# Performance work log

Hardware: AMD Instinct MI355X
Metric: run time of the kernel (lower is better)

Reference implementation:

```python
import jax, jax.numpy as jnp
from jax import lax
import numpy as np

NEG = -1e30  # safe log-space -inf for fp32 (avoids inf-inf NaNs)
EPS = 1e-7   # keras.backend.epsilon()


def setup_inputs() -> dict:
    key = jax.random.key(0)
    k1, k2 = jax.random.split(key)
    B, T, C, L = 512, 512, 96, 64
    y_true = jax.random.randint(k1, (B, L), 0, C - 1, dtype=jnp.int64)  # labels in [0, C-2]
    # y_pred mimics softmax output: positive, rows sum to 1
    logits = jax.random.uniform(k2, (B, T, C), dtype=jnp.float32)
    y_pred = logits / jnp.sum(logits, axis=-1, keepdims=True)
    return {"y_true": y_true, "y_pred": y_pred}


def _ctc_batch_cost(y_true, y_pred):
    # Faithful to keras.backend.ctc_batch_cost with full input/label lengths
    # and blank index = num_classes - 1.
    B, T, C = y_pred.shape
    L = y_true.shape[1]
    blank = C - 1
    S = 2 * L + 1  # extended label length: blanks interleaved

    logp = jnp.log(y_pred + EPS)  # [B, T, C]

    # extended label sequence: blank, l0, blank, l1, ..., blank
    ext = jnp.full((B, S), blank, dtype=y_true.dtype).at[:, 1::2].set(y_true)  # [B, S]

    # log-probs of extended labels at every time step: [T, B, S]
    lp = jnp.take_along_axis(
        logp, jnp.broadcast_to(ext[:, None, :], (B, T, S)), axis=2
    ).transpose(1, 0, 2)

    # skip transition (s-2 -> s) allowed iff ext[s] != blank and ext[s] != ext[s-2]
    skip = jnp.concatenate(
        [jnp.zeros((B, 2), dtype=bool),
         (ext[:, 2:] != blank) & (ext[:, 2:] != ext[:, :-2])],
        axis=1,
    )  # [B, S]

    # init: alpha_0(0) = logp(blank), alpha_0(1) = logp(l0)
    alpha0 = jnp.full((B, S), NEG, dtype=logp.dtype)
    alpha0 = alpha0.at[:, 0].set(lp[0, :, 0]).at[:, 1].set(lp[0, :, 1])

    def step(alpha, lp_t):
        s1 = jnp.pad(alpha[:, :-1], ((0, 0), (1, 0)), constant_values=NEG)
        s2 = jnp.pad(alpha[:, :-2], ((0, 0), (2, 0)), constant_values=NEG)
        a = jnp.logaddexp(alpha, s1)
        a = jnp.where(skip, jnp.logaddexp(a, s2), a)
        return a + lp_t, None

    alpha, _ = lax.scan(step, alpha0, lp[1:])
    loss = -jnp.logaddexp(alpha[:, -1], alpha[:, -2])  # [B]
    return loss[:, None]  # [B, 1], matching ctc_batch_cost


def reference(y_true, y_pred):
    return _ctc_batch_cost(y_true, y_pred)
```

## Files before the change

### kernel.cpp

```cpp
#include <hip/hip_runtime.h>
#include <math.h>


constexpr int Bv = 512;
constexpr int Tv = 512;
constexpr int Cv = 96;
constexpr int Lv = 64;
constexpr int BLANK = Cv - 1;
constexpr float EPSf = 1e-7f;
constexpr int RING = 24;

__device__ __forceinline__ float dpp_wave_shr1(float x) {
    return __int_as_float(
        __builtin_amdgcn_update_dpp(0, __float_as_int(x), 0x138, 0xf, 0xf, true));
}

template <int CTRL>
__device__ __forceinline__ float dpp_maxf(float m) {
    return fmaxf(m, __int_as_float(
        __builtin_amdgcn_update_dpp(0, __float_as_int(m), CTRL, 0xf, 0xf, true)));
}

__global__ void __launch_bounds__(64) ctc_fwd(const int* __restrict__ y_true,
                                              const float* __restrict__ y_pred,
                                              float* __restrict__ out) {
    const int b = blockIdx.x;
    const int l = threadIdx.x;
    const float* __restrict__ yp = y_pred + (size_t)b * (Tv * Cv);

    const int lab   = y_true[b * Lv + l];
    const int labm1 = __shfl_up(lab, 1);
    const bool skip = (l > 0) && (lab != labm1);
    const bool lane0 = (l == 0);

    float a0 = lane0 ? (yp[BLANK] + EPSf) : 0.0f;
    float a1 = lane0 ? (yp[lab]  + EPSf) : 0.0f;
    float a2 = 0.0f;
    int   e_acc = 0;

    float fb[RING], fl[RING];
#pragma unroll
    for (int i = 0; i < RING; ++i) {
        int t = 1 + i;
        fb[i] = yp[t * Cv + BLANK];
        fl[i] = yp[t * Cv + lab];
    }

    auto step = [&](int t, int slot) {
        float pb = fb[slot] + EPSf;
        float pl = fl[slot] + EPSf;
        int tp = t + RING;
        tp = (tp > Tv - 1) ? (Tv - 1) : tp;
        fb[slot] = yp[tp * Cv + BLANK];
        fl[slot] = yp[tp * Cv + lab];

        float a1p = dpp_wave_shr1(a1);
        float na0 = (a0 + a1p) * pb;
        float s1  = a0 + a1 + (skip ? a1p : 0.0f);
        float na1 = s1 * pl;
        float na2 = (a2 + a1) * pb;
        a0 = na0; a1 = na1; a2 = na2;
    };

    auto renorm = [&]() {
        float m = fmaxf(fmaxf(a0, a1), a2);
        m = dpp_maxf<0x111>(m);
        m = dpp_maxf<0x112>(m);
        m = dpp_maxf<0x114>(m);
        m = dpp_maxf<0x118>(m);
        m = dpp_maxf<0x142>(m);
        m = dpp_maxf<0x143>(m);
        float mw = __int_as_float(__builtin_amdgcn_readlane(__float_as_int(m), 63));
        int e;
        (void)frexpf(mw, &e);
        float sc = ldexpf(1.0f, -e);
        a0 *= sc; a1 *= sc; a2 *= sc;
        e_acc += e;
    };

    int t = 1;
    for (int w = 0; w < 21; ++w) {
#pragma unroll
        for (int i = 0; i < RING; ++i, ++t) {
            step(t, i);
            if ((i & 7) == 7) renorm();
        }
    }
#pragma unroll
    for (int i = 0; i < 7; ++i, ++t) step(t, i);

    if (l == 63) {
        float sum = a1 + a2;
        out[b] = -(logf(sum) + (float)e_acc * 0.69314718055994530942f);
    }
}

extern "C" void kernel_launch(void* const* d_in, const int* in_sizes, int n_in,
                              void* d_out, int out_size, void* d_ws, size_t ws_size,
                              hipStream_t stream) {
    const int*   y_true = (const int*)d_in[0];
    const float* y_pred = (const float*)d_in[1];
    float*       out    = (float*)d_out;
    (void)in_sizes; (void)n_in; (void)out_size; (void)d_ws; (void)ws_size;
    ctc_fwd<<<Bv, 64, 0, stream>>>(y_true, y_pred, out);
}
```

Baseline: 164.1 us.

## Stage y_pred chunks into LDS via async global_load_lds double buffering

Replaces the per-lane register ring of strided global loads with bulk asynchronous global-to-LDS copies of 32-row chunks, double-buffered and synchronised with explicit vmcnt waits. Each step then reads its blank and label probabilities from LDS through a small 4-deep register prefetch. This aims to replace scattered 4-byte global gathers with coalesced 16-byte-per-lane transfers and to hide global latency behind the recurrence. In exchange it moves the full 96-class rows (more bytes than the two needed values per row) and depends on hand-coded waitcnt values and on buffer reuse being ordered correctly.

```diff
diff --git a/kernel.cpp b/kernel.cpp
--- a/kernel.cpp
+++ b/kernel.cpp
@@ -8,7 +8,11 @@
 constexpr int Lv = 64;
 constexpr int BLANK = Cv - 1;
 constexpr float EPSf = 1e-7f;
-constexpr int RING = 24;
+
+constexpr int ROWS = 32;
+constexpr int NCHUNK = Tv / ROWS;
+constexpr int CHUNK_FLOATS = ROWS * Cv;
+constexpr int NLOAD = 12;
 
 __device__ __forceinline__ float dpp_wave_shr1(float x) {
     return __int_as_float(
@@ -21,9 +25,21 @@
         __builtin_amdgcn_update_dpp(0, __float_as_int(m), CTRL, 0xf, 0xf, true)));
 }
 
+__device__ __forceinline__ void stage_chunk(const float* g, float* l, int lane) {
+#pragma unroll
+    for (int j = 0; j < NLOAD; ++j) {
+        __builtin_amdgcn_global_load_lds(
+            (const __attribute__((address_space(1))) void*)(g + j * 256 + lane * 4),
+            (__attribute__((address_space(3))) void*)(l + j * 256),
+            16, 0, 0);
+    }
+}
+
 __global__ void __launch_bounds__(64) ctc_fwd(const int* __restrict__ y_true,
                                               const float* __restrict__ y_pred,
                                               float* __restrict__ out) {
+    __shared__ float lds[2 * CHUNK_FLOATS];
+
     const int b = blockIdx.x;
     const int l = threadIdx.x;
     const float* __restrict__ yp = y_pred + (size_t)b * (Tv * Cv);
@@ -33,27 +49,29 @@
     const bool skip = (l > 0) && (lab != labm1);
     const bool lane0 = (l == 0);
 
-    float a0 = lane0 ? (yp[BLANK] + EPSf) : 0.0f;
-    float a1 = lane0 ? (yp[lab]  + EPSf) : 0.0f;
-    float a2 = 0.0f;
-    int   e_acc = 0;
+    stage_chunk(yp, lds, l);
+    stage_chunk(yp + CHUNK_FLOATS, lds + CHUNK_FLOATS, l);
 
-    float fb[RING], fl[RING];
-#pragma unroll
-    for (int i = 0; i < RING; ++i) {
-        int t = 1 + i;
-        fb[i] = yp[t * Cv + BLANK];
-        fl[i] = yp[t * Cv + lab];
-    }
+    float a0 = 0.0f, a1 = 0.0f, a2 = 0.0f;
+    int e_acc = 0;
 
-    auto step = [&](int t, int slot) {
-        float pb = fb[slot] + EPSf;
-        float pl = fl[slot] + EPSf;
-        int tp = t + RING;
-        tp = (tp > Tv - 1) ? (Tv - 1) : tp;
-        fb[slot] = yp[tp * Cv + BLANK];
-        fl[slot] = yp[tp * Cv + lab];
+    float pb0, pl0, pb1, pl1, pb2, pl2, pb3, pl3;
 
+    auto preload4 = [&](const float* buf) {
+        pb0 = buf[0 * Cv + BLANK]; pl0 = buf[0 * Cv + lab];
+        pb1 = buf[1 * Cv + BLANK]; pl1 = buf[1 * Cv + lab];
+        pb2 = buf[2 * Cv + BLANK]; pl2 = buf[2 * Cv + lab];
+        pb3 = buf[3 * Cv + BLANK]; pl3 = buf[3 * Cv + lab];
+    };
+    auto rotload = [&](const float* buf, int rn) {
+        pb0 = pb1; pl0 = pl1;
+        pb1 = pb2; pl1 = pl2;
+        pb2 = pb3; pl2 = pl3;
+        pb3 = buf[rn * Cv + BLANK]; pl3 = buf[rn * Cv + lab];
+    };
+    auto step = [&]() {
+        float pb = pb0 + EPSf;
+        float pl = pl0 + EPSf;
         float a1p = dpp_wave_shr1(a1);
         float na0 = (a0 + a1p) * pb;
         float s1  = a0 + a1 + (skip ? a1p : 0.0f);
@@ -61,7 +79,6 @@
         float na2 = (a2 + a1) * pb;
         a0 = na0; a1 = na1; a2 = na2;
     };
-
     auto renorm = [&]() {
         float m = fmaxf(fmaxf(a0, a1), a2);
         m = dpp_maxf<0x111>(m);
@@ -78,16 +95,45 @@
         e_acc += e;
     };
 
-    int t = 1;
-    for (int w = 0; w < 21; ++w) {
+    __asm__ __volatile__("" ::: "memory");
+    __builtin_amdgcn_s_waitcnt(0x0F7C);
+    __asm__ __volatile__("" ::: "memory");
+    {
+        const float* buf = lds;
+        preload4(buf);
+        a0 = lane0 ? (pb0 + EPSf) : 0.0f;
+        a1 = lane0 ? (pl0 + EPSf) : 0.0f;
+        a2 = 0.0f;
+        rotload(buf, 4);
 #pragma unroll
-        for (int i = 0; i < RING; ++i, ++t) {
-            step(t, i);
-            if ((i & 7) == 7) renorm();
+        for (int r = 1; r < ROWS; ++r) {
+            step();
+            int rn = r + 4; rn = rn > ROWS - 1 ? ROWS - 1 : rn;
+            rotload(buf, rn);
+            if ((r & 7) == 0) renorm();
         }
     }
+    stage_chunk(yp + 2 * CHUNK_FLOATS, lds, l);
+
+    for (int c = 1; c < NCHUNK; ++c) {
+        __asm__ __volatile__("" ::: "memory");
+        if (c == NCHUNK - 1) __builtin_amdgcn_s_waitcnt(0x0F70);
+        else                 __builtin_amdgcn_s_waitcnt(0x0F7C);
+        __asm__ __volatile__("" ::: "memory");
+
+        const float* buf = lds + (c & 1) * CHUNK_FLOATS;
+        preload4(buf);
 #pragma unroll
-    for (int i = 0; i < 7; ++i, ++t) step(t, i);
+        for (int r = 0; r < ROWS; ++r) {
+            step();
+            int rn = r + 4; rn = rn > ROWS - 1 ? ROWS - 1 : rn;
+            rotload(buf, rn);
+            if ((r & 7) == 0) renorm();
+        }
+        if (c + 2 < NCHUNK)
+            stage_chunk(yp + (c + 2) * CHUNK_FLOATS,
+                        lds + (c & 1) * CHUNK_FLOATS, l);
+    }
 
     if (l == 63) {
         float sum = a1 + a2;
```

Measured after the change: 149.8 us. 8.7% less time.

## Stage time-step chunks in double-buffered LDS via coalesced float4 loads

Applied to the files above, without the earlier changes.

Replaces the per-lane scattered global loads of blank and label probabilities with coalesced float4 loads of whole 32-row chunks. Each chunk is staged into a padded, double-buffered LDS tile and then read from LDS per step, and the global load for chunk c+2 is prefetched. Renormalisation is split into a compute half and a deferred apply half so the reduction latency overlaps with the next steps, and the step maths is rewritten with FMAs. The cost is more LDS use and register pressure for the twelve float4 staging registers. There is also no barrier, which the single-wave block makes unnecessary.

```diff
diff --git a/kernel.cpp b/kernel.cpp
--- a/kernel.cpp
+++ b/kernel.cpp
@@ -8,22 +8,28 @@
 constexpr int Lv = 64;
 constexpr int BLANK = Cv - 1;
 constexpr float EPSf = 1e-7f;
-constexpr int RING = 24;
 
-__device__ __forceinline__ float dpp_wave_shr1(float x) {
+constexpr int ROWS = 32;
+constexpr int NCH  = Tv / ROWS;
+constexpr int CF   = ROWS * Cv;
+constexpr int RS   = 100;
+constexpr int LBUF = ROWS * RS;
+
+__device__ __forceinline__ float dpp_shr1(float x) {
     return __int_as_float(
         __builtin_amdgcn_update_dpp(0, __float_as_int(x), 0x138, 0xf, 0xf, true));
 }
-
-template <int CTRL>
-__device__ __forceinline__ float dpp_maxf(float m) {
+template <int C>
+__device__ __forceinline__ float dppmax(float m) {
     return fmaxf(m, __int_as_float(
-        __builtin_amdgcn_update_dpp(0, __float_as_int(m), CTRL, 0xf, 0xf, true)));
+        __builtin_amdgcn_update_dpp(0, __float_as_int(m), C, 0xf, 0xf, true)));
 }
 
 __global__ void __launch_bounds__(64) ctc_fwd(const int* __restrict__ y_true,
                                               const float* __restrict__ y_pred,
                                               float* __restrict__ out) {
+    __shared__ float lds[2 * LBUF];
+
     const int b = blockIdx.x;
     const int l = threadIdx.x;
     const float* __restrict__ yp = y_pred + (size_t)b * (Tv * Cv);
@@ -31,68 +37,113 @@
     const int lab   = y_true[b * Lv + l];
     const int labm1 = __shfl_up(lab, 1);
     const bool skip = (l > 0) && (lab != labm1);
-    const bool lane0 = (l == 0);
 
-    float a0 = lane0 ? (yp[BLANK] + EPSf) : 0.0f;
-    float a1 = lane0 ? (yp[lab]  + EPSf) : 0.0f;
-    float a2 = 0.0f;
+#define WA(i) ((((i)*64 + l) / 24) * 400 + (((i)*64 + l) % 24) * 16)
+    const int wa0 = WA(0),  wa1 = WA(1),  wa2 = WA(2),  wa3 = WA(3);
+    const int wa4 = WA(4),  wa5 = WA(5),  wa6 = WA(6),  wa7 = WA(7);
+    const int wa8 = WA(8),  wa9 = WA(9), wa10 = WA(10), wa11 = WA(11);
+#undef WA
+
+    float4 G0, G1, G2, G3, G4, G5, G6, G7, G8, G9, G10, G11;
+#define GLOAD(g) do { const float* gp_ = (g) + l * 4;                        \
+    G0 = *(const float4*)(gp_ +    0); G1 = *(const float4*)(gp_ +  256);    \
+    G2 = *(const float4*)(gp_ +  512); G3 = *(const float4*)(gp_ +  768);    \
+    G4 = *(const float4*)(gp_ + 1024); G5 = *(const float4*)(gp_ + 1280);    \
+    G6 = *(const float4*)(gp_ + 1536); G7 = *(const float4*)(gp_ + 1792);    \
+    G8 = *(const float4*)(gp_ + 2048); G9 = *(const float4*)(gp_ + 2304);    \
+    G10= *(const float4*)(gp_ + 2560); G11= *(const float4*)(gp_ + 2816); } while (0)
+#define SWRITE(bufn) do { char* p_ = (char*)(bufn);                          \
+    *(float4*)(p_ + wa0) = G0;  *(float4*)(p_ + wa1) = G1;                   \
+    *(float4*)(p_ + wa2) = G2;  *(float4*)(p_ + wa3) = G3;                   \
+    *(float4*)(p_ + wa4) = G4;  *(float4*)(p_ + wa5) = G5;                   \
+    *(float4*)(p_ + wa6) = G6;  *(float4*)(p_ + wa7) = G7;                   \
+    *(float4*)(p_ + wa8) = G8;  *(float4*)(p_ + wa9) = G9;                   \
+    *(float4*)(p_ + wa10)= G10; *(float4*)(p_ + wa11)= G11; } while (0)
+
+    float AB0,AB1,AB2,AB3,AB4,AB5,AB6,AB7, AL0,AL1,AL2,AL3,AL4,AL5,AL6,AL7;
+    float BB0,BB1,BB2,BB3,BB4,BB5,BB6,BB7, BL0,BL1,BL2,BL3,BL4,BL5,BL6,BL7;
+#define LOAD8(P, bb, r0) do { const float* pB_ = (bb) + BLANK;               \
+    const float* pL_ = (bb) + lab;                                           \
+    P##B0 = pB_[((r0)+0)*RS]; P##L0 = pL_[((r0)+0)*RS];                      \
+    P##B1 = pB_[((r0)+1)*RS]; P##L1 = pL_[((r0)+1)*RS];                      \
+    P##B2 = pB_[((r0)+2)*RS]; P##L2 = pL_[((r0)+2)*RS];                      \
+    P##B3 = pB_[((r0)+3)*RS]; P##L3 = pL_[((r0)+3)*RS];                      \
+    P##B4 = pB_[((r0)+4)*RS]; P##L4 = pL_[((r0)+4)*RS];                      \
+    P##B5 = pB_[((r0)+5)*RS]; P##L5 = pL_[((r0)+5)*RS];                      \
+    P##B6 = pB_[((r0)+6)*RS]; P##L6 = pL_[((r0)+6)*RS];                      \
+    P##B7 = pB_[((r0)+7)*RS]; P##L7 = pL_[((r0)+7)*RS]; } while (0)
+
+    float a0, a1, a2;
     int   e_acc = 0;
+    float sc_p = 1.0f; int e_p = 0;
 
-    float fb[RING], fl[RING];
-#pragma unroll
-    for (int i = 0; i < RING; ++i) {
-        int t = 1 + i;
-        fb[i] = yp[t * Cv + BLANK];
-        fl[i] = yp[t * Cv + lab];
-    }
-
-    auto step = [&](int t, int slot) {
-        float pb = fb[slot] + EPSf;
-        float pl = fl[slot] + EPSf;
-        int tp = t + RING;
-        tp = (tp > Tv - 1) ? (Tv - 1) : tp;
-        fb[slot] = yp[tp * Cv + BLANK];
-        fl[slot] = yp[tp * Cv + lab];
-
-        float a1p = dpp_wave_shr1(a1);
-        float na0 = (a0 + a1p) * pb;
-        float s1  = a0 + a1 + (skip ? a1p : 0.0f);
-        float na1 = s1 * pl;
+    auto step = [&](float PB, float PL) {
+        float pb  = PB + EPSf;
+        float pl  = PL + EPSf;
+        float pls = skip ? pl : 0.0f;
+        float a1p = dpp_shr1(a1);
+        float t01 = a0 + a1;
+        float na1 = fmaf(a1p, pls, t01 * pl);
+        float na0 = fmaf(a1p, pb, a0 * pb);
         float na2 = (a2 + a1) * pb;
         a0 = na0; a1 = na1; a2 = na2;
     };
+    auto rn_apply = [&]() {
+        a0 *= sc_p; a1 *= sc_p; a2 *= sc_p; e_acc += e_p;
+    };
+    auto rn_compute = [&]() {
+        float m = fmaxf(fmaxf(a0, a1), a2);
+        m = dppmax<0x111>(m); m = dppmax<0x112>(m); m = dppmax<0x114>(m);
+        m = dppmax<0x118>(m); m = dppmax<0x142>(m); m = dppmax<0x143>(m);
+        float mw = __int_as_float(__builtin_amdgcn_readlane(__float_as_int(m), 63));
+        int e; (void)frexpf(mw, &e);
+        sc_p = ldexpf(1.0f, -e); e_p = e;
+    };
+#define GROUP8(P) do {                                                       \
+    step(P##B0, P##L0); step(P##B1, P##L1); step(P##B2, P##L2);              \
+    step(P##B3, P##L3); rn_apply();                                          \
+    step(P##B4, P##L4); step(P##B5, P##L5); step(P##B6, P##L6);              \
+    step(P##B7, P##L7); rn_compute(); } while (0)
 
-    auto renorm = [&]() {
-        float m = fmaxf(fmaxf(a0, a1), a2);
-        m = dpp_maxf<0x111>(m);
-        m = dpp_maxf<0x112>(m);
-        m = dpp_maxf<0x114>(m);
-        m = dpp_maxf<0x118>(m);
-        m = dpp_maxf<0x142>(m);
-        m = dpp_maxf<0x143>(m);
-        float mw = __int_as_float(__builtin_amdgcn_readlane(__float_as_int(m), 63));
-        int e;
-        (void)frexpf(mw, &e);
-        float sc = ldexpf(1.0f, -e);
-        a0 *= sc; a1 *= sc; a2 *= sc;
-        e_acc += e;
-    };
+    GLOAD(yp);
+    SWRITE(lds);
+    GLOAD(yp + CF);
+    LOAD8(A, lds, 0);
+    const bool lane0 = (l == 0);
+    a0 = lane0 ? (AB0 + EPSf) : 0.0f;
+    a1 = lane0 ? (AL0 + EPSf) : 0.0f;
+    a2 = 0.0f;
 
-    int t = 1;
-    for (int w = 0; w < 21; ++w) {
-#pragma unroll
-        for (int i = 0; i < RING; ++i, ++t) {
-            step(t, i);
-            if ((i & 7) == 7) renorm();
+    for (int c = 0; c < NCH; ++c) {
+        float* bufB = lds + (c & 1) * LBUF;
+        float* bufN = lds + ((c & 1) ^ 1) * LBUF;
+
+        LOAD8(B, bufB, 8);
+        if (c == 0) {
+            step(AB1, AL1); step(AB2, AL2); step(AB3, AL3); rn_apply();
+            step(AB4, AL4); step(AB5, AL5); step(AB6, AL6); step(AB7, AL7);
+            rn_compute();
+        } else {
+            GROUP8(A);
         }
+        LOAD8(A, bufB, 16);
+        GROUP8(B);
+        LOAD8(B, bufB, 24);
+        GROUP8(A);
+        if (c < NCH - 1) SWRITE(bufN);
+        if (c < NCH - 2) GLOAD(yp + (size_t)(c + 2) * CF);
+        if (c < NCH - 1) LOAD8(A, bufN, 0);
+        GROUP8(B);
     }
-#pragma unroll
-    for (int i = 0; i < 7; ++i, ++t) step(t, i);
 
     if (l == 63) {
         float sum = a1 + a2;
         out[b] = -(logf(sum) + (float)e_acc * 0.69314718055994530942f);
     }
+#undef GLOAD
+#undef SWRITE
+#undef LOAD8
+#undef GROUP8
 }
 
 extern "C" void kernel_launch(void* const* d_in, const int* in_sizes, int n_in,
```

New measurement: 148.1 us. 1.11x faster.

## Stream full chunks of y_pred via coalesced float4 loads into an LDS sink

Applied to the files above, without the earlier changes.

Each wavefront now issues coalesced float4 loads covering whole 32-row chunks of y_pred and writes them to a dummy LDS buffer. This pulls the lines into cache ahead of the scattered per-lane gathers of the blank and label probabilities, which are double-buffered in register groups of 8 rows. Renormalization is split into a compute phase and a deferred apply phase and uses exponent bit arithmetic instead of frexpf/ldexpf, so the reduction latency is taken off the critical recurrence. The cost is loading every element of y_pred (mostly unused), extra LDS stores and high register pressure from 24 float4 prefetch registers.

```diff
diff --git a/kernel.cpp b/kernel.cpp
--- a/kernel.cpp
+++ b/kernel.cpp
@@ -8,22 +8,26 @@
 constexpr int Lv = 64;
 constexpr int BLANK = Cv - 1;
 constexpr float EPSf = 1e-7f;
-constexpr int RING = 24;
 
-__device__ __forceinline__ float dpp_wave_shr1(float x) {
+constexpr int ROWS = 32;
+constexpr int NCH  = Tv / ROWS;
+constexpr int CF   = ROWS * Cv;
+
+__device__ __forceinline__ float dpp_shr1(float x) {
     return __int_as_float(
         __builtin_amdgcn_update_dpp(0, __float_as_int(x), 0x138, 0xf, 0xf, true));
 }
-
-template <int CTRL>
-__device__ __forceinline__ float dpp_maxf(float m) {
+template <int C>
+__device__ __forceinline__ float dppmax(float m) {
     return fmaxf(m, __int_as_float(
-        __builtin_amdgcn_update_dpp(0, __float_as_int(m), CTRL, 0xf, 0xf, true)));
+        __builtin_amdgcn_update_dpp(0, __float_as_int(m), C, 0xf, 0xf, true)));
 }
 
 __global__ void __launch_bounds__(64) ctc_fwd(const int* __restrict__ y_true,
                                               const float* __restrict__ y_pred,
                                               float* __restrict__ out) {
+    __shared__ float sink_lds[CF];
+
     const int b = blockIdx.x;
     const int l = threadIdx.x;
     const float* __restrict__ yp = y_pred + (size_t)b * (Tv * Cv);
@@ -31,68 +35,113 @@
     const int lab   = y_true[b * Lv + l];
     const int labm1 = __shfl_up(lab, 1);
     const bool skip = (l > 0) && (lab != labm1);
-    const bool lane0 = (l == 0);
 
-    float a0 = lane0 ? (yp[BLANK] + EPSf) : 0.0f;
-    float a1 = lane0 ? (yp[lab]  + EPSf) : 0.0f;
-    float a2 = 0.0f;
+    const float* __restrict__ gB = yp + BLANK;
+    const float* __restrict__ gL = yp + lab;
+
+    float4 G0,G1,G2,G3,G4,G5,G6,G7,G8,G9,G10,G11;
+    float4 H0,H1,H2,H3,H4,H5,H6,H7,H8,H9,H10,H11;
+#define GLOAD(S, g) do { const float* gp_ = (g) + l * 4;                     \
+    S##0 = *(const float4*)(gp_ +    0); S##1 = *(const float4*)(gp_ +  256);\
+    S##2 = *(const float4*)(gp_ +  512); S##3 = *(const float4*)(gp_ +  768);\
+    S##4 = *(const float4*)(gp_ + 1024); S##5 = *(const float4*)(gp_ + 1280);\
+    S##6 = *(const float4*)(gp_ + 1536); S##7 = *(const float4*)(gp_ + 1792);\
+    S##8 = *(const float4*)(gp_ + 2048); S##9 = *(const float4*)(gp_ + 2304);\
+    S##10= *(const float4*)(gp_ + 2560); S##11= *(const float4*)(gp_ + 2816);\
+    } while (0)
+#define SINK(S) do { float4* sp_ = (float4*)sink_lds + l;                    \
+    sp_[0]   = S##0; sp_[64]  = S##1; sp_[128] = S##2; sp_[192] = S##3;      \
+    sp_[256] = S##4; sp_[320] = S##5; sp_[384] = S##6; sp_[448] = S##7;      \
+    sp_[512] = S##8; sp_[576] = S##9; sp_[640] = S##10; sp_[704] = S##11;    \
+    } while (0)
+
+    GLOAD(G, yp);
+    GLOAD(H, yp + CF);
+
+    float PB0,PB1,PB2,PB3,PB4,PB5,PB6,PB7, PL0,PL1,PL2,PL3,PL4,PL5,PL6,PL7;
+    float QB0,QB1,QB2,QB3,QB4,QB5,QB6,QB7, QL0,QL1,QL2,QL3,QL4,QL5,QL6,QL7;
+#define LOADG(P, g) do {                                                     \
+    const float* pB_ = gB + (size_t)(8 * (g)) * Cv;                          \
+    const float* pL_ = gL + (size_t)(8 * (g)) * Cv;                          \
+    P##B0 = pB_[0*Cv]; P##L0 = pL_[0*Cv]; P##B1 = pB_[1*Cv]; P##L1 = pL_[1*Cv];\
+    P##B2 = pB_[2*Cv]; P##L2 = pL_[2*Cv]; P##B3 = pB_[3*Cv]; P##L3 = pL_[3*Cv];\
+    P##B4 = pB_[4*Cv]; P##L4 = pL_[4*Cv]; P##B5 = pB_[5*Cv]; P##L5 = pL_[5*Cv];\
+    P##B6 = pB_[6*Cv]; P##L6 = pL_[6*Cv]; P##B7 = pB_[7*Cv]; P##L7 = pL_[7*Cv];\
+    } while (0)
+
+    LOADG(P, 0);
+    LOADG(Q, 1);
+
+    float a0, a1, a2;
     int   e_acc = 0;
+    float sc_p = 1.0f; int e_p = 0;
 
-    float fb[RING], fl[RING];
-#pragma unroll
-    for (int i = 0; i < RING; ++i) {
-        int t = 1 + i;
-        fb[i] = yp[t * Cv + BLANK];
-        fl[i] = yp[t * Cv + lab];
-    }
-
-    auto step = [&](int t, int slot) {
-        float pb = fb[slot] + EPSf;
-        float pl = fl[slot] + EPSf;
-        int tp = t + RING;
-        tp = (tp > Tv - 1) ? (Tv - 1) : tp;
-        fb[slot] = yp[tp * Cv + BLANK];
-        fl[slot] = yp[tp * Cv + lab];
-
-        float a1p = dpp_wave_shr1(a1);
+    auto step = [&](float PB, float PL) {
+        float pb  = PB + EPSf;
+        float pl  = PL + EPSf;
+        float a1p = dpp_shr1(a1);
         float na0 = (a0 + a1p) * pb;
         float s1  = a0 + a1 + (skip ? a1p : 0.0f);
         float na1 = s1 * pl;
         float na2 = (a2 + a1) * pb;
         a0 = na0; a1 = na1; a2 = na2;
     };
-
-    auto renorm = [&]() {
+    auto rn_apply = [&]() {
+        a0 *= sc_p; a1 *= sc_p; a2 *= sc_p; e_acc += e_p;
+    };
+    auto rn_compute = [&]() {
         float m = fmaxf(fmaxf(a0, a1), a2);
-        m = dpp_maxf<0x111>(m);
-        m = dpp_maxf<0x112>(m);
-        m = dpp_maxf<0x114>(m);
-        m = dpp_maxf<0x118>(m);
-        m = dpp_maxf<0x142>(m);
-        m = dpp_maxf<0x143>(m);
+        m = dppmax<0x111>(m); m = dppmax<0x112>(m); m = dppmax<0x114>(m);
+        m = dppmax<0x118>(m); m = dppmax<0x142>(m); m = dppmax<0x143>(m);
         float mw = __int_as_float(__builtin_amdgcn_readlane(__float_as_int(m), 63));
-        int e;
-        (void)frexpf(mw, &e);
-        float sc = ldexpf(1.0f, -e);
-        a0 *= sc; a1 *= sc; a2 *= sc;
-        e_acc += e;
+        unsigned ef = __float_as_uint(mw) >> 23;
+        e_p  = (int)ef - 126;
+        sc_p = __uint_as_float((253u - ef) << 23);
     };
 
-    int t = 1;
-    for (int w = 0; w < 21; ++w) {
-#pragma unroll
-        for (int i = 0; i < RING; ++i, ++t) {
-            step(t, i);
-            if ((i & 7) == 7) renorm();
+#define STEP_PF(P, i) do { step(P##B##i, P##L##i);                           \
+    P##B##i = pB2[(i) * Cv]; P##L##i = pL2[(i) * Cv]; } while (0)
+#define GROUP(P, g) do {                                                     \
+    int r20_ = 8 * ((g) + 2); if (r20_ > Tv - 8) r20_ = Tv - 8;              \
+    const float* pB2 = gB + (size_t)r20_ * Cv;                               \
+    const float* pL2 = gL + (size_t)r20_ * Cv;                               \
+    STEP_PF(P,0); STEP_PF(P,1); STEP_PF(P,2); STEP_PF(P,3); rn_apply();      \
+    STEP_PF(P,4); STEP_PF(P,5); STEP_PF(P,6); STEP_PF(P,7); rn_compute();    \
+    } while (0)
+
+    {
+        const bool lane0 = (l == 0);
+        a0 = lane0 ? (PB0 + EPSf) : 0.0f;
+        a1 = lane0 ? (PL0 + EPSf) : 0.0f;
+        a2 = 0.0f;
+        const float* pB2 = gB + (size_t)16 * Cv;
+        const float* pL2 = gL + (size_t)16 * Cv;
+        PB0 = pB2[0]; PL0 = pL2[0];
+        STEP_PF(P,1); STEP_PF(P,2); STEP_PF(P,3); rn_apply();
+        STEP_PF(P,4); STEP_PF(P,5); STEP_PF(P,6); STEP_PF(P,7); rn_compute();
+    }
+
+    SINK(G); GLOAD(G, yp + 2 * CF);
+    GROUP(Q, 1); GROUP(P, 2); GROUP(Q, 3);
+
+    for (int c = 1; c < NCH; ++c) {
+        if (c <= NCH - 3) {
+            if (c & 1) { SINK(H); GLOAD(H, yp + (size_t)(c + 2) * CF); }
+            else       { SINK(G); GLOAD(G, yp + (size_t)(c + 2) * CF); }
         }
+        int g = 4 * c;
+        GROUP(P, g); GROUP(Q, g + 1); GROUP(P, g + 2); GROUP(Q, g + 3);
     }
-#pragma unroll
-    for (int i = 0; i < 7; ++i, ++t) step(t, i);
 
     if (l == 63) {
         float sum = a1 + a2;
         out[b] = -(logf(sum) + (float)e_acc * 0.69314718055994530942f);
     }
+#undef GLOAD
+#undef SINK
+#undef LOADG
+#undef STEP_PF
+#undef GROUP
 }
 
 extern "C" void kernel_launch(void* const* d_in, const int* in_sizes, int n_in,
```

Result: faster. 158.8 us (-3.2%).
